# Kernel optimization log

Measured on AMD Instinct MI355X. Metric: run time of the kernel, lower is better.

Reference implementation:

```python
import jax, jax.numpy as jnp
import numpy as np

# model dims (DeepSeekV2-Lite-like, reduced expert count)
H = 2048      # hidden_dim
NH = 16       # num_heads
NOPE = 128    # qk_nope_head_dim
ROPE = 64     # qk_rope_head_dim (interleaved rotary)
VD = 128      # v_head_dim
QL = 1536     # q_lora_rank
KVL = 512     # kv_lora_rank
E = 8         # num routed experts
TOPK = 2      # num_experts_per_token
MI = 512      # moe_intermediate_dim
SH_I = 2 * MI # num_shared_experts * moe_intermediate_dim
B = 1
S = 2048
T = B * S
EPS = 1e-6
MOE_SCALE = 1.0  # gating_scaling_factor


def setup_inputs() -> dict:
    key = jax.random.key(0)
    ks = jax.random.split(key, 16)
    def w(k, shape):
        return jax.random.normal(k, shape, dtype=jnp.float32) * 0.02
    # interleaved rotary tables: one angle per (even,odd) pair
    half = ROPE // 2
    pos = jnp.arange(S, dtype=jnp.float32)
    inv_freq = 1.0 / (10000.0 ** (jnp.arange(half, dtype=jnp.float32) * 2.0 / ROPE))
    ang = pos[:, None] * inv_freq[None, :]              # [S, half]
    sin = jnp.tile(jnp.sin(ang), (B, 1))                # [T, half]
    cos = jnp.tile(jnp.cos(ang), (B, 1))
    return {
        "x": jax.random.normal(ks[0], (T, H), jnp.float32),
        "skip": jax.random.normal(ks[1], (T, H), jnp.float32),
        "rotary_sin": sin,
        "rotary_cos": cos,
        "ln1_w": jnp.ones((H,), jnp.float32),
        "ln2_w": jnp.ones((H,), jnp.float32),
        "w_qa": w(ks[2], (QL, H)),
        "qa_norm_w": jnp.ones((QL,), jnp.float32),
        "w_qb": w(ks[3], (NH * (NOPE + ROPE), QL)),
        "w_kva": w(ks[4], (KVL + ROPE, H)),
        "kva_norm_w": jnp.ones((KVL,), jnp.float32),
        "w_kb": w(ks[5], (NH * NOPE, KVL)),
        "w_vb": w(ks[6], (NH * VD, KVL)),
        "w_o": w(ks[7], (H, NH * VD)),
        "gate_w": w(ks[8], (E, H)),
        "moe_up_w": w(ks[9], (E, 2 * MI, H)),
        "moe_down_w": w(ks[10], (E, H, MI)),
        "shared_up_w": w(ks[11], (2 * SH_I, H)),
        "shared_down_w": w(ks[12], (H, SH_I)),
        "batch": B,
    }


def _rms(v, w):
    return v * jax.lax.rsqrt(jnp.mean(v * v, axis=-1, keepdims=True) + EPS) * w


def _rope_interleaved(v, sin, cos):
    # v: [T, nh, ROPE]; sin/cos: [T, ROPE//2]; rotate (even, odd) pairs
    x1, x2 = v[..., 0::2], v[..., 1::2]
    s, c = sin[:, None, :], cos[:, None, :]
    o1 = x1 * c - x2 * s
    o2 = x1 * s + x2 * c
    return jnp.stack([o1, o2], axis=-1).reshape(v.shape)


def reference(x, skip, rotary_sin, rotary_cos, ln1_w, ln2_w, w_qa, qa_norm_w,
              w_qb, w_kva, kva_norm_w, w_kb, w_vb, w_o, gate_w,
              moe_up_w, moe_down_w, shared_up_w, shared_down_w, batch):
    Tt = x.shape[0]
    Sq = Tt // batch
    # SkipRMSNorm #1
    x1 = x + skip
    n1 = _rms(x1, ln1_w)
    # ---- MLA attention (prefill path, decoding_batches=0) ----
    qa = _rms(n1 @ w_qa.T, qa_norm_w)                               # [T, QL]
    q = (qa @ w_qb.T).reshape(Tt, NH, NOPE + ROPE)
    q_nope, q_pe = q[..., :NOPE], q[..., NOPE:]
    q_pe = _rope_interleaved(q_pe, rotary_sin, rotary_cos)
    kv = n1 @ w_kva.T                                               # [T, KVL+ROPE]
    ckv = _rms(kv[:, :KVL], kva_norm_w)
    k_pe = _rope_interleaved(kv[:, KVL:][:, None, :], rotary_sin, rotary_cos)  # [T,1,ROPE]
    k_nope = (ckv @ w_kb.T).reshape(Tt, NH, NOPE)
    v = (ckv @ w_vb.T).reshape(Tt, NH, VD)
    qf = jnp.concatenate([q_nope, q_pe], -1).reshape(batch, Sq, NH, NOPE + ROPE)
    kf = jnp.concatenate([k_nope, jnp.broadcast_to(k_pe, (Tt, NH, ROPE))], -1)
    kf = kf.reshape(batch, Sq, NH, NOPE + ROPE)
    vf = v.reshape(batch, Sq, NH, VD)
    scale = 1.0 / np.sqrt(NOPE + ROPE)
    scores = jnp.einsum('bqhd,bkhd->bhqk', qf, kf) * scale
    causal = jnp.tril(jnp.ones((Sq, Sq), bool))
    scores = jnp.where(causal[None, None], scores, jnp.float32(-1e30))
    p = jax.nn.softmax(scores, axis=-1)
    o = jnp.einsum('bhqk,bkhd->bqhd', p, vf).reshape(Tt, NH * VD)
    attn = o @ w_o.T
    # SkipRMSNorm #2
    x2 = x1 + attn
    n2 = _rms(x2, ln2_w)
    # ---- MoE FFN: softmax gate, greedy top-k, normalized probs ----
    probs = jax.nn.softmax(n2 @ gate_w.T, axis=-1)                  # [T, E]
    tv, ti = jax.lax.top_k(probs, TOPK)
    tv = tv / jnp.sum(tv, axis=-1, keepdims=True) * MOE_SCALE
    routed = jnp.zeros_like(n2)
    for e in range(E):  # fixed small expert count; masked dense dispatch
        we = jnp.sum(tv * (ti == e), axis=-1)                       # [T]
        h = n2 @ moe_up_w[e].T                                      # [T, 2*MI]
        h = jax.nn.silu(h[:, :MI]) * h[:, MI:]
        routed = routed + we[:, None] * (h @ moe_down_w[e].T)
    # shared experts (dense swiglu MLP)
    hs = n2 @ shared_up_w.T
    hs = jax.nn.silu(hs[:, :SH_I]) * hs[:, SH_I:]
    ffn = routed + hs @ shared_down_w.T
    return (x2, ffn)
```

## Files before the change

### kernel.cpp

```cpp
#include <hip/hip_runtime.h>
#include <hip/hip_bf16.h>

#define H 2048
#define NH 16
#define NOPE 128
#define ROPE_D 64
#define DQK 192
#define VD 128
#define QL 1536
#define KVL 512
#define NE 8
#define MI_D 512
#define SHI 1024
#define EPS 1e-6f
#define MAXA 5120

typedef unsigned short bfu;
typedef short bf16x8 __attribute__((ext_vector_type(8)));
typedef float f32x4 __attribute__((ext_vector_type(4)));

#define MFMA16(a, b, c) __builtin_amdgcn_mfma_f32_16x16x32_bf16(a, b, c, 0, 0, 0)

#define BAR_PLAIN()   asm volatile("s_barrier" ::: "memory")
#define BAR_LGKM0()   asm volatile("s_waitcnt lgkmcnt(0)\n\ts_barrier" ::: "memory")
#define BAR_VM4()     asm volatile("s_waitcnt vmcnt(4)\n\ts_barrier" ::: "memory")
#define BAR_VM0()     asm volatile("s_waitcnt vmcnt(0)\n\ts_barrier" ::: "memory")

__device__ __forceinline__ float bf2f(bfu u) {
    union { unsigned int i; float f; } w; w.i = ((unsigned int)u) << 16; return w.f;
}
__device__ __forceinline__ bfu f2bf(float f) {
    union { float f; unsigned int i; } u; u.f = f;
    return (bfu)((u.i + 0x7fffu + ((u.i >> 16) & 1u)) >> 16);
}

__device__ __forceinline__ void async16(const bfu* g, bfu* l) {
    __builtin_amdgcn_global_load_lds((const __attribute__((address_space(1))) void*)g,
                                     (__attribute__((address_space(3))) void*)l, 16, 0, 0);
}

__device__ __forceinline__ int xcd_swz(int b, int nt) {
    int q = nt >> 3, r = nt & 7;
    int x = b & 7, o = b >> 3;
    int base = (x < r) ? x * (q + 1) : r * (q + 1) + (x - r) * q;
    return base + o;
}

__device__ __forceinline__ float blk_sum(float v) {
    __shared__ float sb[4];
    for (int o = 32; o > 0; o >>= 1) v += __shfl_down(v, o, 64);
    int lane = threadIdx.x & 63, w = threadIdx.x >> 6;
    __syncthreads();
    if (lane == 0) sb[w] = v;
    __syncthreads();
    return sb[0] + sb[1] + sb[2] + sb[3];
}

struct GemmSeg {
    const bfu* A; const bfu* B; void* C; void* C2;
    const int* aidx; const int* eid;
    long bstride;
    int N, K, ldm3, mode, nx, ntiles;
};

__device__ __forceinline__ void gemm_body(const bfu* __restrict__ A, const bfu* __restrict__ B,
                                          void* __restrict__ Cv, void* __restrict__ Cv2,
                                          int N, int K, int ldm3, int mode,
                                          const int* __restrict__ aidx,
                                          const int* __restrict__ eid, long bstride,
                                          int bx, int by,
                                          bfu* sAb, bfu* sBb) {
    bfu (*sA)[128 * 32] = (bfu (*)[128 * 32])sAb;
    bfu (*sB)[128 * 32] = (bfu (*)[128 * 32])sBb;
    const int tid = threadIdx.x;
    const int lane = tid & 63, w = tid >> 6;
    const int quad = lane >> 4, li = lane & 15;
    const int m0 = by * 128, n0 = bx * 128;
    const bfu* Bp = B + (eid ? (size_t)eid[by] * bstride : 0);

    const int l4 = lane >> 2;
    const int lg = lane & 3;
    const int kc = lg ^ ((lane >> 3) & 3);
    int r0 = m0 + w * 32 + l4, r1 = r0 + 16;
    if (aidx) { r0 = aidx[r0]; r1 = aidx[r1]; }
    const bfu* gA0 = A + (size_t)r0 * K + kc * 8;
    const bfu* gA1 = A + (size_t)r1 * K + kc * 8;
    const bfu* gB0 = Bp + (size_t)(n0 + w * 32 + l4) * K + kc * 8;
    const bfu* gB1 = gB0 + (size_t)16 * K;
    const int oA0 = (w * 32) * 32, oA1 = (w * 32 + 16) * 32;

    const int wm = (w >> 1) * 64, wn = (w & 1) * 64;
    const int fg = (quad ^ ((li >> 1) & 3)) * 8;
    int oa[4], ob[4];
#pragma unroll
    for (int t4 = 0; t4 < 4; ++t4) {
        oa[t4] = (wm + t4 * 16 + li) * 32 + fg;
        ob[t4] = (wn + t4 * 16 + li) * 32 + fg;
    }
    f32x4 acc[4][4];
#pragma unroll
    for (int i = 0; i < 4; ++i)
#pragma unroll
        for (int j = 0; j < 4; ++j) acc[i][j] = (f32x4){0.f, 0.f, 0.f, 0.f};

    const int nb = K / 32;
    async16(gA0, &sA[0][oA0]); async16(gA1, &sA[0][oA1]);
    async16(gB0, &sB[0][oA0]); async16(gB1, &sB[0][oA1]);
    async16(gA0 + 32, &sA[1][oA0]); async16(gA1 + 32, &sA[1][oA1]);
    async16(gB0 + 32, &sB[1][oA0]); async16(gB1 + 32, &sB[1][oA1]);

    int cur = 0;
    for (int it = 0; it < nb; ++it) {
        if (it < nb - 1) { BAR_VM4(); } else { BAR_VM0(); }
        bf16x8 av[4], bv[4];
#pragma unroll
        for (int t4 = 0; t4 < 4; ++t4) av[t4] = *(const bf16x8*)&sA[cur][oa[t4]];
#pragma unroll
        for (int t4 = 0; t4 < 4; ++t4) bv[t4] = *(const bf16x8*)&sB[cur][ob[t4]];
        if (it + 2 < nb) {
            const int k1 = (it + 2) * 32;
            int nxt = cur + 2; if (nxt >= 3) nxt -= 3;
            async16(gA0 + k1, &sA[nxt][oA0]); async16(gA1 + k1, &sA[nxt][oA1]);
            async16(gB0 + k1, &sB[nxt][oA0]); async16(gB1 + k1, &sB[nxt][oA1]);
        }
#pragma unroll
        for (int mt = 0; mt < 4; ++mt)
#pragma unroll
            for (int nt = 0; nt < 4; ++nt)
                acc[mt][nt] = MFMA16(av[mt], bv[nt], acc[mt][nt]);
        if (++cur >= 3) cur = 0;
    }

    if (mode == 4 && n0 >= 2048) {
        __syncthreads();
        const int ST = 136;
#pragma unroll
        for (int mt = 0; mt < 4; ++mt)
#pragma unroll
            for (int nt = 0; nt < 4; ++nt)
#pragma unroll
                for (int r = 0; r < 4; ++r) {
                    int lm = wm + mt * 16 + quad * 4 + r;
                    int ln = wn + nt * 16 + li;
                    bfu* p = (ln < 90) ? (sAb + ln * ST) : (sBb + (ln - 90) * ST);
                    p[lm] = f2bf(acc[mt][nt][r]);
                }
        __syncthreads();
        bfu* C2 = (bfu*)Cv2 + (size_t)(n0 - 2048) * ldm3 + m0;
        int li16 = tid & 15, ng = tid >> 4;
#pragma unroll
        for (int nn = 0; nn < 8; ++nn) {
            int n = ng + nn * 16;
            const bfu* p = (n < 90) ? (sAb + n * ST) : (sBb + (n - 90) * ST);
            bf16x8 v = *(const bf16x8*)(p + li16 * 8);
            *(bf16x8*)(C2 + (size_t)n * ldm3 + li16 * 8) = v;
        }
        return;
    }

#pragma unroll
    for (int mt = 0; mt < 4; ++mt)
#pragma unroll
        for (int nt = 0; nt < 4; ++nt) {
            int row = m0 + wm + mt * 16 + quad * 4;
            int col = n0 + wn + nt * 16 + li;
            if (mode == 0) {
                float* C = (float*)Cv;
#pragma unroll
                for (int r = 0; r < 4; ++r) C[(size_t)(row + r) * N + col] = acc[mt][nt][r];
            } else if (mode == 1) {
                bfu* C = (bfu*)Cv;
#pragma unroll
                for (int r = 0; r < 4; ++r) C[(size_t)(row + r) * N + col] = f2bf(acc[mt][nt][r]);
            } else {
                bfu* C = (bfu*)Cv;
#pragma unroll
                for (int r = 0; r < 4; ++r) C[(size_t)(row + r) * 2048 + col] = f2bf(acc[mt][nt][r]);
            }
        }
}

__global__ __launch_bounds__(256) void gemm_multi(GemmSeg s0, GemmSeg s1) {
    __shared__ bfu sA[3][128 * 32];
    __shared__ bfu sB[3][128 * 32];
    int b = blockIdx.x;
    if (b < s0.ntiles) {
        int wg = xcd_swz(b, s0.ntiles);
        int ny = s0.ntiles / s0.nx;
        gemm_body(s0.A, s0.B, s0.C, s0.C2, s0.N, s0.K, s0.ldm3, s0.mode,
                  s0.aidx, s0.eid, s0.bstride, wg / ny, wg % ny, &sA[0][0], &sB[0][0]);
    } else {
        int lb = b - s0.ntiles;
        int wg = xcd_swz(lb, s1.ntiles);
        int ny = s1.ntiles / s1.nx;
        gemm_body(s1.A, s1.B, s1.C, s1.C2, s1.N, s1.K, s1.ldm3, s1.mode,
                  s1.aidx, s1.eid, s1.bstride, wg / ny, wg % ny, &sA[0][0], &sB[0][0]);
    }
}

struct CastArgs {
    const float* s[10];
    bfu* d[10];
    unsigned start[11];
    int pad[10];
};
__global__ __launch_bounds__(256) void k_cast_all(CastArgs a) {
    unsigned base = blockIdx.x * 1024 + threadIdx.x;
#pragma unroll
    for (int j = 0; j < 4; ++j) {
        unsigned g = base + j * 256;
        if (g >= a.start[10]) return;
        int id = 0;
#pragma unroll
        for (int i = 1; i < 10; ++i) if (g >= a.start[i]) id = i;
        size_t i4 = (size_t)(g - a.start[id]) * 4;
        ushort4 u = {0, 0, 0, 0};
        if (!a.pad[id] || (i4 >> 11) < 576) {
            float4 x = *(const float4*)(a.s[id] + i4);
            u.x = f2bf(x.x); u.y = f2bf(x.y); u.z = f2bf(x.z); u.w = f2bf(x.w);
        }
        *(ushort4*)(a.d[id] + i4) = u;
    }
}

__global__ __launch_bounds__(256) void k_add_rms(const float* __restrict__ x, const float* __restrict__ skip,
                                                 const float* __restrict__ w,
                                                 float* __restrict__ x1, bfu* __restrict__ n1b) {
    int t = blockIdx.x;
    size_t base = (size_t)t * H;
    float loc[8]; float ss = 0.f;
#pragma unroll
    for (int i = 0; i < 8; ++i) {
        int c = threadIdx.x + i * 256;
        float v = x[base + c] + skip[base + c];
        loc[i] = v; ss += v * v;
        x1[base + c] = v;
    }
    float tot = blk_sum(ss);
    float r = rsqrtf(tot / (float)H + EPS);
#pragma unroll
    for (int i = 0; i < 8; ++i) {
        int c = threadIdx.x + i * 256;
        n1b[base + c] = f2bf(loc[i] * r * w[c]);
    }
}

__global__ __launch_bounds__(256) void k_qkv_post(const bfu* __restrict__ qkv,
                                                  const float* __restrict__ qa_nw,
                                                  const float* __restrict__ kva_nw,
                                                  const float* __restrict__ sin_, const float* __restrict__ cos_,
                                                  bfu* __restrict__ qab, bfu* __restrict__ ckv,
                                                  bfu* __restrict__ kpe) {
    int t = blockIdx.x;
    const bfu* row = qkv + (size_t)t * 2176;
    float qa[6]; float ss1 = 0.f;
#pragma unroll
    for (int i = 0; i < 6; ++i) {
        float v = bf2f(row[threadIdx.x + i * 256]); qa[i] = v; ss1 += v * v;
    }
    float v0 = bf2f(row[1536 + threadIdx.x]), v1 = bf2f(row[1792 + threadIdx.x]);
    float s1 = blk_sum(ss1);
    float s2 = blk_sum(v0 * v0 + v1 * v1);
    float r1 = rsqrtf(s1 / (float)QL + EPS);
    float r2 = rsqrtf(s2 / 512.f + EPS);
#pragma unroll
    for (int i = 0; i < 6; ++i) {
        int c = threadIdx.x + i * 256;
        qab[(size_t)t * QL + c] = f2bf(qa[i] * r1 * qa_nw[c]);
    }
    ckv[(size_t)t * 512 + threadIdx.x]       = f2bf(v0 * r2 * kva_nw[threadIdx.x]);
    ckv[(size_t)t * 512 + threadIdx.x + 256] = f2bf(v1 * r2 * kva_nw[threadIdx.x + 256]);
    if (threadIdx.x < 32) {
        int p = threadIdx.x;
        float x1v = bf2f(row[2048 + 2 * p]), x2v = bf2f(row[2048 + 2 * p + 1]);
        float s = sin_[t * 32 + p], c = cos_[t * 32 + p];
        kpe[(size_t)t * 64 + 2 * p]     = f2bf(x1v * c - x2v * s);
        kpe[(size_t)t * 64 + 2 * p + 1] = f2bf(x1v * s + x2v * c);
    }
}

__global__ __launch_bounds__(256) void k_flash_mfma(const bfu* __restrict__ qb,
                                                    const bfu* __restrict__ kn,
                                                    const bfu* __restrict__ kpe,
                                                    const bfu* __restrict__ vt,
                                                    bfu* __restrict__ O,
                                                    const float* __restrict__ rsin,
                                                    const float* __restrict__ rcos, int T) {
    __shared__ bfu Ks[64 * 200];
    __shared__ bfu VtL[2][128 * 40];
    __shared__ bfu P[64 * 72];
    const int tid = threadIdx.x;
    const int lane = tid & 63, w = tid >> 6;
    const int quad = lane >> 4, li = lane & 15;
    const int q0 = ((int)gridDim.x - 1 - (int)blockIdx.x) * 64;
    const int h = blockIdx.y;
    const float scale = 0.07216878364870322f;

    bf16x8 qf[6];
    {
        int qrow = q0 + w * 16 + li;
        const bfu* qp = qb + ((size_t)qrow * NH + h) * DQK;
#pragma unroll
        for (int s6 = 0; s6 < 6; ++s6) {
            bf16x8 v = *(const bf16x8*)(qp + s6 * 32 + quad * 8);
            if (s6 >= 4) {
                int pb = (s6 - 4) * 16 + quad * 4;
#pragma unroll
                for (int j = 0; j < 4; ++j) {
                    float x1 = bf2f((bfu)v[2 * j]), x2 = bf2f((bfu)v[2 * j + 1]);
                    float s = rsin[qrow * 32 + pb + j], c = rcos[qrow * 32 + pb + j];
                    v[2 * j]     = (short)f2bf(x1 * c - x2 * s);
                    v[2 * j + 1] = (short)f2bf(x1 * s + x2 * c);
                }
            }
            qf[s6] = v;
        }
    }
    f32x4 accO[8];
#pragma unroll
    for (int i = 0; i < 8; ++i) accO[i] = (f32x4){0.f, 0.f, 0.f, 0.f};
    float lrow[4] = {0.f, 0.f, 0.f, 0.f};

    int kr[6], kg[6];
#pragma unroll
    for (int it = 0; it < 6; ++it) { int G = tid + it * 256; kr[it] = G / 24; kg[it] = G % 24; }
    int vn[4], vgl[4], vkc[4];
#pragma unroll
    for (int it = 0; it < 4; ++it) {
        int idx = tid + it * 256; vn[it] = idx >> 3; vgl[it] = idx & 7;
        vkc[it] = (vgl[it] & 4) | ((vgl[it] & 3) ^ ((vn[it] >> 1) & 3));
    }
    bf16x8 kreg[6], vreg[4];
#pragma unroll
    for (int it = 0; it < 6; ++it)
        kreg[it] = (kg[it] < 16) ? *(const bf16x8*)(kn + (size_t)kr[it] * (NH * 128) + h * 128 + kg[it] * 8)
                                 : *(const bf16x8*)(kpe + (size_t)kr[it] * 64 + (kg[it] - 16) * 8);
#pragma unroll
    for (int it = 0; it < 4; ++it)
        vreg[it] = *(const bf16x8*)(vt + (size_t)(h * 128 + vn[it]) * T + vkc[it] * 8);

    const int fgv = (quad ^ ((li >> 1) & 3)) * 8;
    const int kend = q0 + 64;
    for (int k0 = 0; k0 < kend; k0 += 64) {
        BAR_PLAIN();
#pragma unroll
        for (int it = 0; it < 6; ++it) *(bf16x8*)(Ks + kr[it] * 200 + kg[it] * 8) = kreg[it];
#pragma unroll
        for (int it = 0; it < 4; ++it)
            *(bf16x8*)(VtL[vgl[it] >> 2] + vn[it] * 40 + (vgl[it] & 3) * 8) = vreg[it];
        if (k0 + 64 < kend) {
            int k1 = k0 + 64;
#pragma unroll
            for (int it = 0; it < 6; ++it)
                kreg[it] = (kg[it] < 16) ? *(const bf16x8*)(kn + (size_t)(k1 + kr[it]) * (NH * 128) + h * 128 + kg[it] * 8)
                                         : *(const bf16x8*)(kpe + (size_t)(k1 + kr[it]) * 64 + (kg[it] - 16) * 8);
#pragma unroll
            for (int it = 0; it < 4; ++it)
                vreg[it] = *(const bf16x8*)(vt + (size_t)(h * 128 + vn[it]) * T + k1 + vkc[it] * 8);
        }
        BAR_LGKM0();
        f32x4 s[4];
#pragma unroll
        for (int ct = 0; ct < 4; ++ct) {
            f32x4 a = (f32x4){0.f, 0.f, 0.f, 0.f};
#pragma unroll
            for (int s6 = 0; s6 < 6; ++s6) {
                bf16x8 kf = *(const bf16x8*)(Ks + (ct * 16 + li) * 200 + s6 * 32 + quad * 8);
                a = MFMA16(qf[s6], kf, a);
            }
            s[ct] = a;
        }
#pragma unroll
        for (int ct = 0; ct < 4; ++ct)
#pragma unroll
            for (int r = 0; r < 4; ++r) {
                int row = q0 + w * 16 + quad * 4 + r;
                float p = (k0 + ct * 16 + li <= row) ? __expf(s[ct][r] * scale) : 0.f;
                s[ct][r] = p;
                lrow[r] += p;
            }
#pragma unroll
        for (int ct = 0; ct < 4; ++ct)
#pragma unroll
            for (int r = 0; r < 4; ++r)
                P[(w * 16 + quad * 4 + r) * 72 + ct * 16 + li] = f2bf(s[ct][r]);
        bf16x8 pf[2];
#pragma unroll
        for (int ks = 0; ks < 2; ++ks)
            pf[ks] = *(const bf16x8*)(P + (w * 16 + li) * 72 + ks * 32 + quad * 8);
#pragma unroll
        for (int v8 = 0; v8 < 8; ++v8)
#pragma unroll
            for (int ks = 0; ks < 2; ++ks) {
                bf16x8 vf = *(const bf16x8*)(VtL[ks] + (v8 * 16 + li) * 40 + fgv);
                accO[v8] = MFMA16(pf[ks], vf, accO[v8]);
            }
    }
#pragma unroll
    for (int r = 0; r < 4; ++r) {
        float l = lrow[r];
        l += __shfl_xor(l, 1); l += __shfl_xor(l, 2);
        l += __shfl_xor(l, 4); l += __shfl_xor(l, 8);
        lrow[r] = 1.0f / l;
    }
#pragma unroll
    for (int v8 = 0; v8 < 8; ++v8)
#pragma unroll
        for (int r = 0; r < 4; ++r) {
            float val = accO[v8][r] * lrow[r];
            O[(size_t)(q0 + w * 16 + quad * 4 + r) * (NH * 128) + h * 128 + v8 * 16 + li] = f2bf(val);
        }
}

__global__ __launch_bounds__(256) void k_x2_n2(const float* __restrict__ x1, const bfu* __restrict__ attn,
                                               const float* __restrict__ ln2w, float* __restrict__ outx2,
                                               bfu* __restrict__ n2b, const float* __restrict__ gw,
                                               int* __restrict__ eidx, float* __restrict__ wts,
                                               int* __restrict__ cnt) {
    int t = blockIdx.x;
    size_t base = (size_t)t * H;
    float loc[8]; float ss = 0.f;
#pragma unroll
    for (int i = 0; i < 8; ++i) {
        int c = threadIdx.x + i * 256;
        float vv = x1[base + c] + bf2f(attn[base + c]);
        loc[i] = vv; ss += vv * vv;
        outx2[base + c] = vv;
    }
    float tot = blk_sum(ss);
    float r = rsqrtf(tot / (float)H + EPS);
    float pe[NE] = {0.f, 0.f, 0.f, 0.f, 0.f, 0.f, 0.f, 0.f};
#pragma unroll
    for (int i = 0; i < 8; ++i) {
        int c = threadIdx.x + i * 256;
        float nv = loc[i] * r * ln2w[c];
        n2b[base + c] = f2bf(nv);
#pragma unroll
        for (int e = 0; e < NE; ++e) pe[e] += nv * gw[e * H + c];
    }
    __shared__ float sred[4][NE];
    int lane = threadIdx.x & 63, wv = threadIdx.x >> 6;
#pragma unroll
    for (int e = 0; e < NE; ++e) {
        float v = pe[e];
        for (int o = 32; o > 0; o >>= 1) v += __shfl_down(v, o, 64);
        if (lane == 0) sred[wv][e] = v;
    }
    __syncthreads();
    if (threadIdx.x == 0) {
        float logits[NE];
        float m = -1e30f;
        for (int e = 0; e < NE; ++e) {
            logits[e] = sred[0][e] + sred[1][e] + sred[2][e] + sred[3][e];
            m = fmaxf(m, logits[e]);
        }
        float p[NE];
        for (int e = 0; e < NE; ++e) p[e] = __expf(logits[e] - m);
        int i1 = 0;
        for (int e = 1; e < NE; ++e) if (p[e] > p[i1]) i1 = e;
        int i2 = -1;
        for (int e = 0; e < NE; ++e) if (e != i1 && (i2 < 0 || p[e] > p[i2])) i2 = e;
        float denom = p[i1] + p[i2];
        eidx[t * 2] = i1; eidx[t * 2 + 1] = i2;
        wts[t * 2] = p[i1] / denom; wts[t * 2 + 1] = p[i2] / denom;
        atomicAdd(&cnt[i1], 1); atomicAdd(&cnt[i2], 1);
    }
}

__global__ __launch_bounds__(256) void k_moe_init(int* __restrict__ cnt, int* __restrict__ slot,
                                                  int* __restrict__ eid, int* __restrict__ idx,
                                                  float* __restrict__ aw) {
    int tid = threadIdx.x;
    if (tid < NE) { cnt[tid] = 0; slot[tid] = 0; }
    if (tid < 40) eid[tid] = 0;
    for (int i = tid; i < MAXA; i += 256) { idx[i] = 0; aw[i] = 0.f; }
}

__global__ __launch_bounds__(64) void k_moe_scan(const int* __restrict__ cnt, int* __restrict__ base,
                                                 int* __restrict__ eid) {
    if (threadIdx.x == 0) {
        int off = 0;
        for (int e = 0; e < NE; ++e) {
            base[e] = off;
            int nb = (cnt[e] + 127) >> 7;
            for (int j = 0; j < nb; ++j) eid[(off >> 7) + j] = e;
            off += nb << 7;
        }
    }
}

__global__ __launch_bounds__(256) void k_moe_scatter(const int* __restrict__ eidx, const float* __restrict__ wts,
                                                     const int* __restrict__ base, int* __restrict__ slot,
                                                     int* __restrict__ idx, float* __restrict__ aw,
                                                     int* __restrict__ posmap) {
    int t = blockIdx.x * 256 + threadIdx.x;
#pragma unroll
    for (int j = 0; j < 2; ++j) {
        int e = eidx[t * 2 + j];
        int p = base[e] + atomicAdd(&slot[e], 1);
        idx[p] = t; aw[p] = wts[t * 2 + j]; posmap[t * 2 + j] = p;
    }
}

__global__ __launch_bounds__(256) void k_silu_both(const bfu* __restrict__ hsh, bfu* __restrict__ gsh,
                                                   const bfu* __restrict__ hsp, const float* __restrict__ aw,
                                                   bfu* __restrict__ gsp, int T) {
    int b = blockIdx.x;
    if (b < T) {
        const bfu* row = hsh + (size_t)b * 2048;
        bfu* grow = gsh + (size_t)b * 1024;
#pragma unroll
        for (int j = 0; j < 4; ++j) {
            int i = threadIdx.x + j * 256;
            float a = bf2f(row[i]), bb = bf2f(row[1024 + i]);
            grow[i] = f2bf(a / (1.0f + __expf(-a)) * bb);
        }
    } else {
        int row = b - T;
        float we = aw[row];
        const bfu* hr = hsp + (size_t)row * 1024;
        bfu* gr = gsp + (size_t)row * 512;
#pragma unroll
        for (int j = 0; j < 2; ++j) {
            int i = threadIdx.x + j * 256;
            float a = bf2f(hr[i]), bb = bf2f(hr[512 + i]);
            gr[i] = f2bf(we * a / (1.0f + __expf(-a)) * bb);
        }
    }
}

__global__ __launch_bounds__(256) void k_ffn_out(const float* __restrict__ routed, const bfu* __restrict__ dsp,
                                                 const int* __restrict__ posmap, float* __restrict__ out,
                                                 size_t TH) {
    int t = blockIdx.x;
    int p1 = posmap[t * 2], p2 = posmap[t * 2 + 1];
    const bfu* d1 = dsp + (size_t)p1 * H;
    const bfu* d2 = dsp + (size_t)p2 * H;
#pragma unroll
    for (int j = 0; j < 8; ++j) {
        int c = threadIdx.x + j * 256;
        out[TH + (size_t)t * H + c] = routed[(size_t)t * H + c] + bf2f(d1[c]) + bf2f(d2[c]);
    }
}

static inline GemmSeg mk_seg(const bfu* A, const bfu* B, void* C, void* C2,
                             const int* aidx, const int* eid, long bstride,
                             int N, int K, int ldm3, int mode, int nx, int ny) {
    GemmSeg s;
    s.A = A; s.B = B; s.C = C; s.C2 = C2; s.aidx = aidx; s.eid = eid; s.bstride = bstride;
    s.N = N; s.K = K; s.ldm3 = ldm3; s.mode = mode; s.nx = nx; s.ntiles = nx * ny;
    return s;
}

extern "C" void kernel_launch(void* const* d_in, const int* in_sizes, int n_in,
                              void* d_out, int out_size, void* d_ws, size_t ws_size,
                              hipStream_t stream) {
    const float* x      = (const float*)d_in[0];
    const float* skip   = (const float*)d_in[1];
    const float* rsin   = (const float*)d_in[2];
    const float* rcos   = (const float*)d_in[3];
    const float* ln1w   = (const float*)d_in[4];
    const float* ln2w   = (const float*)d_in[5];
    const float* w_qa   = (const float*)d_in[6];
    const float* qa_nw  = (const float*)d_in[7];
    const float* w_qb   = (const float*)d_in[8];
    const float* w_kva  = (const float*)d_in[9];
    const float* kva_nw = (const float*)d_in[10];
    const float* w_kb   = (const float*)d_in[11];
    const float* w_vb   = (const float*)d_in[12];
    const float* w_o    = (const float*)d_in[13];
    const float* gate_w = (const float*)d_in[14];
    const float* mup    = (const float*)d_in[15];
    const float* mdown  = (const float*)d_in[16];
    const float* shup   = (const float*)d_in[17];
    const float* shdown = (const float*)d_in[18];

    const int T = in_sizes[0] / H;

    bfu* WB = (bfu*)d_ws;
    bfu* wqkv_b  = WB + 0;
    bfu* wkbv_b  = WB + 4456448;
    bfu* wqb_b   = WB + 6553600;
    bfu* wo_b    = WB + 11272192;
    bfu* mup_b   = WB + 15466496;
    bfu* mdown_b = WB + 32243712;
    bfu* shup_b  = WB + 40632320;
    bfu* shdn_b  = WB + 44826624;
    const size_t WBYTES = 93847552;

    char* AB = (char*)d_ws + WBYTES;
    float* x1f    = (float*)(AB + 0);
    float* routed = (float*)(AB + 0);
    bfu*   n1b    = (bfu*)(AB + 16777216);
    bfu*   qkvb   = (bfu*)(AB + 25165824);
    bfu*   knb    = (bfu*)(AB + 25165824);
    bfu*   hsp    = (bfu*)(AB + 25165824);
    bfu*   qab    = (bfu*)(AB + 35651584);
    bfu*   gsp    = (bfu*)(AB + 35651584);
    bfu*   qbb    = (bfu*)(AB + 41943040);
    bfu*   attnb  = (bfu*)(AB + 41943040);
    bfu*   ckvb   = (bfu*)(AB + 54525952);
    bfu*   kpeb   = (bfu*)(AB + 56623104);
    char*  G      = AB + 56885248;
    int*   eidx   = (int*)(G);
    float* wts    = (float*)(G + 16384);
    int*   posmap = (int*)(G + 32768);
    int*   midx   = (int*)(G + 49152);
    float* maw    = (float*)(G + 69632);
    int*   mcnt   = (int*)(G + 90112);
    int*   mbase  = (int*)(G + 90112 + 64);
    int*   mslot  = (int*)(G + 90112 + 128);
    int*   meid   = (int*)(G + 90112 + 192);
    bfu*   ob     = (bfu*)(AB + 57016320);
    bfu*   gsb    = (bfu*)(AB + 57016320);
    bfu*   vtb    = (bfu*)(AB + 65404928);
    bfu*   hsb    = (bfu*)(AB + 65404928);
    bfu*   dsp    = (bfu*)(AB + 65404928);
    const size_t REQ = WBYTES + 86376448;
    if (ws_size < REQ) return;

    {
        CastArgs ca;
        const float* ss[10] = {w_qa, w_kva, w_kb, w_vb, w_qb, w_o, mup, mdown, shup, shdown};
        bfu* dd[10] = {wqkv_b, wqkv_b + 3145728, wkbv_b, wkbv_b + 1048576, wqb_b,
                       wo_b, mup_b, mdown_b, shup_b, shdn_b};
        unsigned n4[10] = {786432, 327680, 262144, 262144, 1179648, 1048576, 4194304, 2097152, 1048576, 524288};
        unsigned acc = 0;
        for (int i = 0; i < 10; ++i) { ca.s[i] = ss[i]; ca.d[i] = dd[i]; ca.start[i] = acc; acc += n4[i]; ca.pad[i] = (i == 1); }
        ca.start[10] = acc;
        k_cast_all<<<(acc + 1023) / 1024, 256, 0, stream>>>(ca);
    }

    k_add_rms<<<T, 256, 0, stream>>>(x, skip, ln1w, x1f, n1b);
    {
        GemmSeg s = mk_seg(n1b, wqkv_b, qkvb, nullptr, nullptr, nullptr, 0, 2176, H, 0, 1, 2176 / 128, T / 128);
        gemm_multi<<<s.ntiles, 256, 0, stream>>>(s, s);
    }
    k_qkv_post<<<T, 256, 0, stream>>>(qkvb, qa_nw, kva_nw, rsin, rcos, qab, ckvb, kpeb);
    {
        GemmSeg sq = mk_seg(qab, wqb_b, qbb, nullptr, nullptr, nullptr, 0, NH * DQK, QL, 0, 1, (NH * DQK) / 128, T / 128);
        GemmSeg sk = mk_seg(ckvb, wkbv_b, knb, vtb, nullptr, nullptr, 0, 4096, KVL, T, 4, 4096 / 128, T / 128);
        gemm_multi<<<sq.ntiles + sk.ntiles, 256, 0, stream>>>(sq, sk);
    }
    k_flash_mfma<<<dim3(T / 64, NH), 256, 0, stream>>>(qbb, knb, kpeb, vtb, ob, rsin, rcos, T);
    {
        GemmSeg s = mk_seg(ob, wo_b, attnb, nullptr, nullptr, nullptr, 0, H, NH * VD, 0, 1, H / 128, T / 128);
        gemm_multi<<<s.ntiles, 256, 0, stream>>>(s, s);
    }
    k_moe_init<<<1, 256, 0, stream>>>(mcnt, mslot, meid, midx, maw);
    k_x2_n2<<<T, 256, 0, stream>>>(x1f, attnb, ln2w, (float*)d_out, n1b, gate_w, eidx, wts, mcnt);
    k_moe_scan<<<1, 64, 0, stream>>>(mcnt, mbase, meid);
    k_moe_scatter<<<T / 256, 256, 0, stream>>>(eidx, wts, mbase, mslot, midx, maw, posmap);
    {
        GemmSeg ssh = mk_seg(n1b, shup_b, hsb, nullptr, nullptr, nullptr, 0, 2048, H, 0, 1, 2048 / 128, T / 128);
        GemmSeg smo = mk_seg(n1b, mup_b, hsp, nullptr, midx, meid, (long)1024 * H, 1024, H, 0, 1, 1024 / 128, MAXA / 128);
        gemm_multi<<<ssh.ntiles + smo.ntiles, 256, 0, stream>>>(ssh, smo);
    }
    k_silu_both<<<T + MAXA, 256, 0, stream>>>(hsb, gsb, hsp, maw, gsp, T);
    {
        GemmSeg ssd = mk_seg(gsb, shdn_b, routed, nullptr, nullptr, nullptr, 0, H, SHI, 0, 0, H / 128, T / 128);
        GemmSeg smd = mk_seg(gsp, mdown_b, dsp, nullptr, nullptr, meid, (long)H * MI_D, H, MI_D, 0, 1, H / 128, MAXA / 128);
        gemm_multi<<<ssd.ntiles + smd.ntiles, 256, 0, stream>>>(ssd, smd);
    }
    k_ffn_out<<<T, 256, 0, stream>>>(routed, dsp, posmap, (float*)d_out, (size_t)T * H);
}
```

Measured before the change: 659.0 us.

## Fuse fp32 weight-to-bf16 conversion into GEMM B-tile loads, drop cast kernel

Removes the separate weight cast kernel and its bf16 weight buffers. Each GEMM now reads fp32 weights directly into registers, packs them to bf16 with v_cvt_pk_bf16_f32, and writes them to a double-buffered LDS tile, with row splitting and zero padding handled inline. This avoids a full write and re-read of about 94 MB of bf16 weights per call. In exchange the GEMMs read twice as many weight bytes and lose the async direct-to-LDS path for B, which weakens latency hiding and changes the barrier and wait structure.

```diff
diff --git a/kernel.cpp b/kernel.cpp
--- a/kernel.cpp
+++ b/kernel.cpp
@@ -23,8 +23,9 @@
 
 #define BAR_PLAIN()   asm volatile("s_barrier" ::: "memory")
 #define BAR_LGKM0()   asm volatile("s_waitcnt lgkmcnt(0)\n\ts_barrier" ::: "memory")
-#define BAR_VM4()     asm volatile("s_waitcnt vmcnt(4)\n\ts_barrier" ::: "memory")
-#define BAR_VM0()     asm volatile("s_waitcnt vmcnt(0)\n\ts_barrier" ::: "memory")
+#define BAR_VM8L0()   asm volatile("s_waitcnt vmcnt(8) lgkmcnt(0)\n\ts_barrier" ::: "memory")
+#define BAR_VM2L0()   asm volatile("s_waitcnt vmcnt(2) lgkmcnt(0)\n\ts_barrier" ::: "memory")
+#define BAR_VM0L0()   asm volatile("s_waitcnt vmcnt(0) lgkmcnt(0)\n\ts_barrier" ::: "memory")
 
 __device__ __forceinline__ float bf2f(bfu u) {
     union { unsigned int i; float f; } w; w.i = ((unsigned int)u) << 16; return w.f;
@@ -32,6 +33,9 @@
 __device__ __forceinline__ bfu f2bf(float f) {
     union { float f; unsigned int i; } u; u.f = f;
     return (bfu)((u.i + 0x7fffu + ((u.i >> 16) & 1u)) >> 16);
+}
+__device__ __forceinline__ unsigned pk2(float lo, float hi) {
+    unsigned r; asm("v_cvt_pk_bf16_f32 %0, %1, %2" : "=v"(r) : "v"(lo), "v"(hi)); return r;
 }
 
 __device__ __forceinline__ void async16(const bfu* g, bfu* l) {
@@ -57,15 +61,18 @@
 }
 
 struct GemmSeg {
-    const bfu* A; const bfu* B; void* C; void* C2;
+    const bfu* A; const float* B0; const float* B1; void* C; void* C2;
     const int* aidx; const int* eid;
     long bstride;
-    int N, K, ldm3, mode, nx, ntiles;
+    int N, K, ldm3, mode, nx, ntiles, nsplit, npad;
 };
 
-__device__ __forceinline__ void gemm_body(const bfu* __restrict__ A, const bfu* __restrict__ B,
+__device__ __forceinline__ void gemm_body(const bfu* __restrict__ A,
+                                          const float* __restrict__ B0f,
+                                          const float* __restrict__ B1f,
                                           void* __restrict__ Cv, void* __restrict__ Cv2,
                                           int N, int K, int ldm3, int mode,
+                                          int nsplit, int npad,
                                           const int* __restrict__ aidx,
                                           const int* __restrict__ eid, long bstride,
                                           int bx, int by,
@@ -76,18 +83,28 @@
     const int lane = tid & 63, w = tid >> 6;
     const int quad = lane >> 4, li = lane & 15;
     const int m0 = by * 128, n0 = bx * 128;
-    const bfu* Bp = B + (eid ? (size_t)eid[by] * bstride : 0);
 
     const int l4 = lane >> 2;
-    const int lg = lane & 3;
-    const int kc = lg ^ ((lane >> 3) & 3);
+    const int kc = (lane & 3) ^ ((lane >> 3) & 3);
     int r0 = m0 + w * 32 + l4, r1 = r0 + 16;
     if (aidx) { r0 = aidx[r0]; r1 = aidx[r1]; }
     const bfu* gA0 = A + (size_t)r0 * K + kc * 8;
     const bfu* gA1 = A + (size_t)r1 * K + kc * 8;
-    const bfu* gB0 = Bp + (size_t)(n0 + w * 32 + l4) * K + kc * 8;
-    const bfu* gB1 = gB0 + (size_t)16 * K;
     const int oA0 = (w * 32) * 32, oA1 = (w * 32 + 16) * 32;
+
+    const int rb0 = n0 + w * 32 + l4, rb1 = rb0 + 16;
+    bool z0 = false, z1 = false;
+    const float* bp0;
+    const float* bp1;
+    if (eid) {
+        const float* Be = B0f + (size_t)eid[by] * bstride;
+        bp0 = Be + (size_t)rb0 * K + kc * 8;
+        bp1 = Be + (size_t)rb1 * K + kc * 8;
+    } else {
+        z0 = rb0 >= npad; z1 = rb1 >= npad;
+        bp0 = ((rb0 < nsplit) ? B0f + (size_t)rb0 * K : B1f + (size_t)(rb0 - nsplit) * K) + kc * 8;
+        bp1 = ((rb1 < nsplit) ? B0f + (size_t)rb1 * K : B1f + (size_t)(rb1 - nsplit) * K) + kc * 8;
+    }
 
     const int wm = (w >> 1) * 64, wn = (w & 1) * 64;
     const int fg = (quad ^ ((li >> 1) & 3)) * 8;
@@ -104,32 +121,60 @@
         for (int j = 0; j < 4; ++j) acc[i][j] = (f32x4){0.f, 0.f, 0.f, 0.f};
 
     const int nb = K / 32;
+    float4 r00, r01, r10, r11;
+#define LOADB(kt) do {                                                          \
+        const float* q0_ = bp0 + (size_t)(kt) * 32;                             \
+        const float* q1_ = bp1 + (size_t)(kt) * 32;                             \
+        if (!z0) { r00 = *(const float4*)q0_; r01 = *(const float4*)(q0_ + 4); }\
+        else { r00 = (float4){0.f,0.f,0.f,0.f}; r01 = (float4){0.f,0.f,0.f,0.f}; } \
+        if (!z1) { r10 = *(const float4*)q1_; r11 = *(const float4*)(q1_ + 4); }\
+        else { r10 = (float4){0.f,0.f,0.f,0.f}; r11 = (float4){0.f,0.f,0.f,0.f}; } \
+    } while (0)
+#define WRITEB(sl) do {                                                         \
+        uint4 w0_, w1_;                                                         \
+        w0_.x = pk2(r00.x, r00.y); w0_.y = pk2(r00.z, r00.w);                   \
+        w0_.z = pk2(r01.x, r01.y); w0_.w = pk2(r01.z, r01.w);                   \
+        w1_.x = pk2(r10.x, r10.y); w1_.y = pk2(r10.z, r10.w);                   \
+        w1_.z = pk2(r11.x, r11.y); w1_.w = pk2(r11.z, r11.w);                   \
+        *(uint4*)&sB[sl][oA0 + lane * 8] = w0_;                                 \
+        *(uint4*)&sB[sl][oA1 + lane * 8] = w1_;                                 \
+    } while (0)
+
+    LOADB(0);
     async16(gA0, &sA[0][oA0]); async16(gA1, &sA[0][oA1]);
-    async16(gB0, &sB[0][oA0]); async16(gB1, &sB[0][oA1]);
     async16(gA0 + 32, &sA[1][oA0]); async16(gA1 + 32, &sA[1][oA1]);
-    async16(gB0 + 32, &sB[1][oA0]); async16(gB1 + 32, &sB[1][oA1]);
-
-    int cur = 0;
+    WRITEB(0);
+    LOADB(1);
+
+    int curA = 0;
     for (int it = 0; it < nb; ++it) {
-        if (it < nb - 1) { BAR_VM4(); } else { BAR_VM0(); }
+        BAR_PLAIN();
+        if (it + 1 < nb) WRITEB((it + 1) & 1);
+        if (it + 2 < nb) {
+            LOADB(it + 2);
+            const int k1 = (it + 2) * 32;
+            int nxt = curA + 2; if (nxt >= 3) nxt -= 3;
+            async16(gA0 + k1, &sA[nxt][oA0]); async16(gA1 + k1, &sA[nxt][oA1]);
+            BAR_VM8L0();
+        } else if (it + 1 < nb) {
+            BAR_VM2L0();
+        } else {
+            BAR_VM0L0();
+        }
         bf16x8 av[4], bv[4];
 #pragma unroll
-        for (int t4 = 0; t4 < 4; ++t4) av[t4] = *(const bf16x8*)&sA[cur][oa[t4]];
-#pragma unroll
-        for (int t4 = 0; t4 < 4; ++t4) bv[t4] = *(const bf16x8*)&sB[cur][ob[t4]];
-        if (it + 2 < nb) {
-            const int k1 = (it + 2) * 32;
-            int nxt = cur + 2; if (nxt >= 3) nxt -= 3;
-            async16(gA0 + k1, &sA[nxt][oA0]); async16(gA1 + k1, &sA[nxt][oA1]);
-            async16(gB0 + k1, &sB[nxt][oA0]); async16(gB1 + k1, &sB[nxt][oA1]);
-        }
+        for (int t4 = 0; t4 < 4; ++t4) av[t4] = *(const bf16x8*)&sA[curA][oa[t4]];
+#pragma unroll
+        for (int t4 = 0; t4 < 4; ++t4) bv[t4] = *(const bf16x8*)&sB[it & 1][ob[t4]];
 #pragma unroll
         for (int mt = 0; mt < 4; ++mt)
 #pragma unroll
             for (int nt = 0; nt < 4; ++nt)
                 acc[mt][nt] = MFMA16(av[mt], bv[nt], acc[mt][nt]);
-        if (++cur >= 3) cur = 0;
-    }
+        if (++curA >= 3) curA = 0;
+    }
+#undef LOADB
+#undef WRITEB
 
     if (mode == 4 && n0 >= 2048) {
         __syncthreads();
@@ -182,44 +227,21 @@
 
 __global__ __launch_bounds__(256) void gemm_multi(GemmSeg s0, GemmSeg s1) {
     __shared__ bfu sA[3][128 * 32];
-    __shared__ bfu sB[3][128 * 32];
+    __shared__ bfu sB[2][128 * 32];
     int b = blockIdx.x;
     if (b < s0.ntiles) {
         int wg = xcd_swz(b, s0.ntiles);
         int ny = s0.ntiles / s0.nx;
-        gemm_body(s0.A, s0.B, s0.C, s0.C2, s0.N, s0.K, s0.ldm3, s0.mode,
-                  s0.aidx, s0.eid, s0.bstride, wg / ny, wg % ny, &sA[0][0], &sB[0][0]);
+        gemm_body(s0.A, s0.B0, s0.B1, s0.C, s0.C2, s0.N, s0.K, s0.ldm3, s0.mode,
+                  s0.nsplit, s0.npad, s0.aidx, s0.eid, s0.bstride,
+                  wg / ny, wg % ny, &sA[0][0], &sB[0][0]);
     } else {
         int lb = b - s0.ntiles;
         int wg = xcd_swz(lb, s1.ntiles);
         int ny = s1.ntiles / s1.nx;
-        gemm_body(s1.A, s1.B, s1.C, s1.C2, s1.N, s1.K, s1.ldm3, s1.mode,
-                  s1.aidx, s1.eid, s1.bstride, wg / ny, wg % ny, &sA[0][0], &sB[0][0]);
-    }
-}
-
-struct CastArgs {
-    const float* s[10];
-    bfu* d[10];
-    unsigned start[11];
-    int pad[10];
-};
-__global__ __launch_bounds__(256) void k_cast_all(CastArgs a) {
-    unsigned base = blockIdx.x * 1024 + threadIdx.x;
-#pragma unroll
-    for (int j = 0; j < 4; ++j) {
-        unsigned g = base + j * 256;
-        if (g >= a.start[10]) return;
-        int id = 0;
-#pragma unroll
-        for (int i = 1; i < 10; ++i) if (g >= a.start[i]) id = i;
-        size_t i4 = (size_t)(g - a.start[id]) * 4;
-        ushort4 u = {0, 0, 0, 0};
-        if (!a.pad[id] || (i4 >> 11) < 576) {
-            float4 x = *(const float4*)(a.s[id] + i4);
-            u.x = f2bf(x.x); u.y = f2bf(x.y); u.z = f2bf(x.z); u.w = f2bf(x.w);
-        }
-        *(ushort4*)(a.d[id] + i4) = u;
+        gemm_body(s1.A, s1.B0, s1.B1, s1.C, s1.C2, s1.N, s1.K, s1.ldm3, s1.mode,
+                  s1.nsplit, s1.npad, s1.aidx, s1.eid, s1.bstride,
+                  wg / ny, wg % ny, &sA[0][0], &sB[0][0]);
     }
 }
 
@@ -543,12 +565,14 @@
     }
 }
 
-static inline GemmSeg mk_seg(const bfu* A, const bfu* B, void* C, void* C2,
+static inline GemmSeg mk_seg(const bfu* A, const float* B0, const float* B1, void* C, void* C2,
                              const int* aidx, const int* eid, long bstride,
-                             int N, int K, int ldm3, int mode, int nx, int ny) {
+                             int N, int K, int ldm3, int mode, int nx, int ny,
+                             int nsplit, int npad) {
     GemmSeg s;
-    s.A = A; s.B = B; s.C = C; s.C2 = C2; s.aidx = aidx; s.eid = eid; s.bstride = bstride;
-    s.N = N; s.K = K; s.ldm3 = ldm3; s.mode = mode; s.nx = nx; s.ntiles = nx * ny;
+    s.A = A; s.B0 = B0; s.B1 = B1; s.C = C; s.C2 = C2; s.aidx = aidx; s.eid = eid;
+    s.bstride = bstride; s.N = N; s.K = K; s.ldm3 = ldm3; s.mode = mode;
+    s.nx = nx; s.ntiles = nx * ny; s.nsplit = nsplit; s.npad = npad;
     return s;
 }
 
@@ -577,18 +601,7 @@
 
     const int T = in_sizes[0] / H;
 
-    bfu* WB = (bfu*)d_ws;
-    bfu* wqkv_b  = WB + 0;
-    bfu* wkbv_b  = WB + 4456448;
-    bfu* wqb_b   = WB + 6553600;
-    bfu* wo_b    = WB + 11272192;
-    bfu* mup_b   = WB + 15466496;
-    bfu* mdown_b = WB + 32243712;
-    bfu* shup_b  = WB + 40632320;
-    bfu* shdn_b  = WB + 44826624;
-    const size_t WBYTES = 93847552;
-
-    char* AB = (char*)d_ws + WBYTES;
+    char* AB = (char*)d_ws;
     float* x1f    = (float*)(AB + 0);
     float* routed = (float*)(AB + 0);
     bfu*   n1b    = (bfu*)(AB + 16777216);
@@ -616,35 +629,27 @@
     bfu*   vtb    = (bfu*)(AB + 65404928);
     bfu*   hsb    = (bfu*)(AB + 65404928);
     bfu*   dsp    = (bfu*)(AB + 65404928);
-    const size_t REQ = WBYTES + 86376448;
+    const size_t REQ = 86376448;
     if (ws_size < REQ) return;
-
-    {
-        CastArgs ca;
-        const float* ss[10] = {w_qa, w_kva, w_kb, w_vb, w_qb, w_o, mup, mdown, shup, shdown};
-        bfu* dd[10] = {wqkv_b, wqkv_b + 3145728, wkbv_b, wkbv_b + 1048576, wqb_b,
-                       wo_b, mup_b, mdown_b, shup_b, shdn_b};
-        unsigned n4[10] = {786432, 327680, 262144, 262144, 1179648, 1048576, 4194304, 2097152, 1048576, 524288};
-        unsigned acc = 0;
-        for (int i = 0; i < 10; ++i) { ca.s[i] = ss[i]; ca.d[i] = dd[i]; ca.start[i] = acc; acc += n4[i]; ca.pad[i] = (i == 1); }
-        ca.start[10] = acc;
-        k_cast_all<<<(acc + 1023) / 1024, 256, 0, stream>>>(ca);
-    }
 
     k_add_rms<<<T, 256, 0, stream>>>(x, skip, ln1w, x1f, n1b);
     {
-        GemmSeg s = mk_seg(n1b, wqkv_b, qkvb, nullptr, nullptr, nullptr, 0, 2176, H, 0, 1, 2176 / 128, T / 128);
+        GemmSeg s = mk_seg(n1b, w_qa, w_kva, qkvb, nullptr, nullptr, nullptr, 0,
+                           2176, H, 0, 1, 2176 / 128, T / 128, 1536, 2112);
         gemm_multi<<<s.ntiles, 256, 0, stream>>>(s, s);
     }
     k_qkv_post<<<T, 256, 0, stream>>>(qkvb, qa_nw, kva_nw, rsin, rcos, qab, ckvb, kpeb);
     {
-        GemmSeg sq = mk_seg(qab, wqb_b, qbb, nullptr, nullptr, nullptr, 0, NH * DQK, QL, 0, 1, (NH * DQK) / 128, T / 128);
-        GemmSeg sk = mk_seg(ckvb, wkbv_b, knb, vtb, nullptr, nullptr, 0, 4096, KVL, T, 4, 4096 / 128, T / 128);
+        GemmSeg sq = mk_seg(qab, w_qb, w_qb, qbb, nullptr, nullptr, nullptr, 0,
+                            NH * DQK, QL, 0, 1, (NH * DQK) / 128, T / 128, NH * DQK, NH * DQK);
+        GemmSeg sk = mk_seg(ckvb, w_kb, w_vb, knb, vtb, nullptr, nullptr, 0,
+                            4096, KVL, T, 4, 4096 / 128, T / 128, 2048, 4096);
         gemm_multi<<<sq.ntiles + sk.ntiles, 256, 0, stream>>>(sq, sk);
     }
     k_flash_mfma<<<dim3(T / 64, NH), 256, 0, stream>>>(qbb, knb, kpeb, vtb, ob, rsin, rcos, T);
     {
-        GemmSeg s = mk_seg(ob, wo_b, attnb, nullptr, nullptr, nullptr, 0, H, NH * VD, 0, 1, H / 128, T / 128);
+        GemmSeg s = mk_seg(ob, w_o, w_o, attnb, nullptr, nullptr, nullptr, 0,
+                           H, NH * VD, 0, 1, H / 128, T / 128, H, H);
         gemm_multi<<<s.ntiles, 256, 0, stream>>>(s, s);
     }
     k_moe_init<<<1, 256, 0, stream>>>(mcnt, mslot, meid, midx, maw);
@@ -652,14 +657,18 @@
     k_moe_scan<<<1, 64, 0, stream>>>(mcnt, mbase, meid);
     k_moe_scatter<<<T / 256, 256, 0, stream>>>(eidx, wts, mbase, mslot, midx, maw, posmap);
     {
-        GemmSeg ssh = mk_seg(n1b, shup_b, hsb, nullptr, nullptr, nullptr, 0, 2048, H, 0, 1, 2048 / 128, T / 128);
-        GemmSeg smo = mk_seg(n1b, mup_b, hsp, nullptr, midx, meid, (long)1024 * H, 1024, H, 0, 1, 1024 / 128, MAXA / 128);
+        GemmSeg ssh = mk_seg(n1b, shup, shup, hsb, nullptr, nullptr, nullptr, 0,
+                             2048, H, 0, 1, 2048 / 128, T / 128, 2048, 2048);
+        GemmSeg smo = mk_seg(n1b, mup, mup, hsp, nullptr, midx, meid, (long)1024 * H,
+                             1024, H, 0, 1, 1024 / 128, MAXA / 128, 1024, 1024);
         gemm_multi<<<ssh.ntiles + smo.ntiles, 256, 0, stream>>>(ssh, smo);
     }
     k_silu_both<<<T + MAXA, 256, 0, stream>>>(hsb, gsb, hsp, maw, gsp, T);
     {
-        GemmSeg ssd = mk_seg(gsb, shdn_b, routed, nullptr, nullptr, nullptr, 0, H, SHI, 0, 0, H / 128, T / 128);
-        GemmSeg smd = mk_seg(gsp, mdown_b, dsp, nullptr, nullptr, meid, (long)H * MI_D, H, MI_D, 0, 1, H / 128, MAXA / 128);
+        GemmSeg ssd = mk_seg(gsb, shdown, shdown, routed, nullptr, nullptr, nullptr, 0,
+                             H, SHI, 0, 0, H / 128, T / 128, H, H);
+        GemmSeg smd = mk_seg(gsp, mdown, mdown, dsp, nullptr, nullptr, meid, (long)H * MI_D,
+                             H, MI_D, 0, 1, H / 128, MAXA / 128, H, H);
         gemm_multi<<<ssd.ntiles + smd.ntiles, 256, 0, stream>>>(ssd, smd);
     }
     k_ffn_out<<<T, 256, 0, stream>>>(routed, dsp, posmap, (float*)d_out, (size_t)T * H);
```

Result: slower. 731.8 us (+11.0%).
